# Kernel tuning notes

Measured on AMD Instinct MI355X. Metric: run time of the kernel, lower is better.

Reference implementation:

```python
import jax, jax.numpy as jnp
import numpy as np

B, N, D, H, E = 128, 256, 256, 8, 524288
RATIO = 0.5
HD = D // H
K_SEL = int(N * RATIO)  # nodes kept per graph


def setup_inputs() -> dict:
    key = jax.random.key(0)
    ks = jax.random.split(key, 12)
    embeddings = jax.random.normal(ks[0], (B, N, D), dtype=jnp.float32)
    mask = jnp.ones((B, N), dtype=bool)
    dist = jax.random.uniform(ks[1], (B, N, N), dtype=jnp.float32)
    # within-graph random edges, offset per graph
    epg = E // B
    src = jax.random.randint(ks[2], (B, epg), 0, N)
    dst = jax.random.randint(ks[3], (B, epg), 0, N)
    off = (jnp.arange(B) * N)[:, None]
    edge_index = jnp.stack([(src + off).reshape(-1), (dst + off).reshape(-1)]).astype(jnp.int64)
    batch = jnp.repeat(jnp.arange(B, dtype=jnp.int64), N)
    s = 1.0 / np.sqrt(D)
    Wq = jax.random.normal(ks[4], (D, D), jnp.float32) * s
    Wk = jax.random.normal(ks[5], (D, D), jnp.float32) * s
    Wv = jax.random.normal(ks[6], (D, D), jnp.float32) * s
    Wo = jax.random.normal(ks[7], (D, D), jnp.float32) * s
    bq = jnp.zeros((D,), jnp.float32)
    bk = jnp.zeros((D,), jnp.float32)
    bv = jnp.zeros((D,), jnp.float32)
    bo = jnp.zeros((D,), jnp.float32)
    pool_w = jax.random.normal(ks[8], (D,), jnp.float32) * s
    return dict(embeddings=embeddings, mask=mask, dist=dist, edge_index=edge_index,
                batch=batch, Wq=Wq, bq=bq, Wk=Wk, bk=bk, Wv=Wv, bv=bv, Wo=Wo, bo=bo,
                pool_w=pool_w)


def _mha(x, mask, dist, Wq, bq, Wk, bk, Wv, bv, Wo, bo):
    # x: [B,N,D]; dist used as additive attention bias; mask: [B,N] key mask
    q = (x @ Wq + bq).reshape(B, N, H, HD).transpose(0, 2, 1, 3)  # bhnd
    k = (x @ Wk + bk).reshape(B, N, H, HD).transpose(0, 2, 1, 3)
    v = (x @ Wv + bv).reshape(B, N, H, HD).transpose(0, 2, 1, 3)
    scores = jnp.einsum('bhnd,bhmd->bhnm', q, k) / jnp.sqrt(jnp.float32(HD))
    scores = scores + dist[:, None]  # broadcast bias over heads
    scores = jnp.where(mask[:, None, None, :], scores, jnp.float32(-1e9))
    attn = jax.nn.softmax(scores, axis=-1)
    out = jnp.einsum('bhnm,bhmd->bhnd', attn, v)
    out = out.transpose(0, 2, 1, 3).reshape(B, N, D)
    return out @ Wo + bo


def reference(embeddings, mask, dist, edge_index, batch, Wq, bq, Wk, bk, Wv, bv, Wo, bo, pool_w):
    encoder_result = _mha(embeddings, mask, dist, Wq, bq, Wk, bk, Wv, bv, Wo, bo)
    # encoder_result[mask] -> sparse node features; mask is all-true so shape is [B*N, D]
    x = encoder_result.reshape(B * N, D)

    # ---- TopKPooling (PyG semantics): score = x.w/||w||, keep top ceil(ratio*N)/graph ----
    score = (x @ pool_w) / jnp.linalg.norm(pool_w)          # [B*N]
    vals, idx = jax.lax.top_k(score.reshape(B, N), K_SEL)    # per-graph top-k
    perm = (idx + (jnp.arange(B) * N)[:, None]).reshape(-1)  # [B*K] global node ids
    sub_x = x[perm] * jnp.tanh(vals).reshape(-1, 1)
    sub_batch = batch[perm]

    # relabel nodes: new id = position in perm (PyG ordering); dropped -> sentinel
    n_keep = B * K_SEL
    sentinel = n_keep
    new_id = jnp.full((B * N,), sentinel, dtype=edge_index.dtype).at[perm].set(
        jnp.arange(n_keep, dtype=edge_index.dtype))
    row = new_id[edge_index[0]]
    col = new_id[edge_index[1]]
    valid = (row < sentinel) & (col < sentinel)
    row = jnp.where(valid, row, sentinel)
    col = jnp.where(valid, col, sentinel)
    # sort_edge_index: row-major sort; invalid (sentinel) edges pushed to the end
    order = jnp.argsort(row * (sentinel + 1) + col)
    sub_edge_index = jnp.stack([row, col])[:, order]
    return encoder_result, sub_x, sub_edge_index, sub_batch
```

## Files before the change

### kernel.cpp

```cpp
#include <hip/hip_runtime.h>
#include <math.h>

#define Bg   128
#define Ng   256
#define Dg   256
#define Hg   8
#define HDg  32
#define Eg   524288
#define Kg   128
#define BNg  32768
#define SENT 16384

using bf16x8 = __attribute__((ext_vector_type(8))) short;
using f32x4  = __attribute__((ext_vector_type(4))) float;

__device__ inline void split2(float x, short &h, short &l) {
    unsigned u = __float_as_uint(x);
    h = (short)(u >> 16);
    float hf = __uint_as_float(u & 0xffff0000u);
    float r = x - hf;
    l = (short)(__float_as_uint(r) >> 16);
}
__device__ inline unsigned packsplit(float x) {
    unsigned u = __float_as_uint(x);
    float hf = __uint_as_float(u & 0xffff0000u);
    float r = x - hf;
    unsigned lu = __float_as_uint(r);
    return (u >> 16) | (lu & 0xffff0000u);
}
__device__ inline unsigned pack2(short a, short b) {
    return (unsigned)(unsigned short)a | ((unsigned)(unsigned short)b << 16);
}

__global__ __launch_bounds__(256) void split_x(
    const float* __restrict__ x, short* __restrict__ xh, short* __restrict__ xl)
{
    size_t i = ((size_t)blockIdx.x * 256 + threadIdx.x) * 8;
    float4 a = *(const float4*)(x + i);
    float4 b = *(const float4*)(x + i + 4);
    float v[8] = {a.x,a.y,a.z,a.w,b.x,b.y,b.z,b.w};
    short h[8], l[8];
    #pragma unroll
    for (int j = 0; j < 8; ++j) split2(v[j], h[j], l[j]);
    uint4 uh, ul;
    uh.x = pack2(h[0],h[1]); uh.y = pack2(h[2],h[3]);
    uh.z = pack2(h[4],h[5]); uh.w = pack2(h[6],h[7]);
    ul.x = pack2(l[0],l[1]); ul.y = pack2(l[2],l[3]);
    ul.z = pack2(l[4],l[5]); ul.w = pack2(l[6],l[7]);
    *(uint4*)(xh + i) = uh;
    *(uint4*)(xl + i) = ul;
}

__global__ __launch_bounds__(256) void wprep(
    const float* __restrict__ Wq, const float* __restrict__ Wk,
    const float* __restrict__ Wv, const float* __restrict__ Wo,
    short* __restrict__ WTh, short* __restrict__ WTl)
{
    __shared__ float t[64][65];
    const int bid = blockIdx.x;
    const int mat = bid >> 4;
    const int kt = (bid >> 2) & 3, nt = bid & 3;
    const float* W = (mat==0) ? Wq : (mat==1) ? Wk : (mat==2) ? Wv : Wo;
    const int tid = threadIdx.x;
    const int r = tid >> 2, c4 = tid & 3;
    #pragma unroll
    for (int i = 0; i < 4; ++i) {
        float4 v = *(const float4*)(W + (size_t)(kt*64 + r)*256 + nt*64 + c4*16 + i*4);
        t[r][c4*16 + i*4 + 0] = v.x; t[r][c4*16 + i*4 + 1] = v.y;
        t[r][c4*16 + i*4 + 2] = v.z; t[r][c4*16 + i*4 + 3] = v.w;
    }
    __syncthreads();
    const int n = r, k0 = c4 * 16;
    short hb[16], lb[16];
    #pragma unroll
    for (int i = 0; i < 16; ++i) split2(t[k0 + i][n], hb[i], lb[i]);
    size_t base = (size_t)mat*65536 + (size_t)(nt*64 + n)*256 + kt*64 + k0;
    uint4 uh0, uh1, ul0, ul1;
    uh0.x=pack2(hb[0],hb[1]);  uh0.y=pack2(hb[2],hb[3]);  uh0.z=pack2(hb[4],hb[5]);  uh0.w=pack2(hb[6],hb[7]);
    uh1.x=pack2(hb[8],hb[9]);  uh1.y=pack2(hb[10],hb[11]);uh1.z=pack2(hb[12],hb[13]);uh1.w=pack2(hb[14],hb[15]);
    ul0.x=pack2(lb[0],lb[1]);  ul0.y=pack2(lb[2],lb[3]);  ul0.z=pack2(lb[4],lb[5]);  ul0.w=pack2(lb[6],lb[7]);
    ul1.x=pack2(lb[8],lb[9]);  ul1.y=pack2(lb[10],lb[11]);ul1.z=pack2(lb[12],lb[13]);ul1.w=pack2(lb[14],lb[15]);
    *(uint4*)&WTh[base]     = uh0; *(uint4*)&WTh[base + 8] = uh1;
    *(uint4*)&WTl[base]     = ul0; *(uint4*)&WTl[base + 8] = ul1;
}

__global__ __launch_bounds__(256) void qkv_mm(
    const short* __restrict__ xh, const short* __restrict__ xl,
    const short* __restrict__ WTh, const short* __restrict__ WTl,
    const float* __restrict__ bq, const float* __restrict__ bk, const float* __restrict__ bv,
    unsigned* __restrict__ Qp, unsigned* __restrict__ Kp, unsigned* __restrict__ Vp)
{
    const int z = blockIdx.z;
    const float* bias = (z==0) ? bq : (z==1) ? bk : bv;
    unsigned* out     = (z==0) ? Qp : (z==1) ? Kp : Vp;
    const float scale = (z==0) ? 0.17677669529663687f : 1.0f;
    const short* bth = WTh + (size_t)z * 65536;
    const short* btl = WTl + (size_t)z * 65536;
    __shared__ __align__(16) short lds[16384];
    const int tid = threadIdx.x;
    const int lane = tid & 63, w = tid >> 6;
    const int g = lane >> 4, li = lane & 15;
    const int wr = w >> 1, wc = w & 1;
    const int m0 = blockIdx.x * 128, n0 = blockIdx.y * 128;
    f32x4 acc[4][4];
    #pragma unroll
    for (int i = 0; i < 4; ++i)
        #pragma unroll
        for (int j = 0; j < 4; ++j) acc[i][j] = (f32x4){0.f,0.f,0.f,0.f};

    for (int k0 = 0; k0 < 256; k0 += 32) {
        #pragma unroll
        for (int it = 0; it < 2; ++it) {
            int chunk = it*256 + tid;
            int r = chunk >> 2, c = chunk & 3;
            size_t ga = (size_t)(m0 + r)*256 + k0 + c*8;
            size_t gb = (size_t)(n0 + r)*256 + k0 + c*8;
            uint4 vh = *(const uint4*)(xh + ga);
            uint4 vl = *(const uint4*)(xl + ga);
            uint4 wh = *(const uint4*)(bth + gb);
            uint4 wl = *(const uint4*)(btl + gb);
            *(uint4*)&lds[        chunk*8] = vh;
            *(uint4*)&lds[ 4096 + chunk*8] = vl;
            *(uint4*)&lds[ 8192 + chunk*8] = wh;
            *(uint4*)&lds[12288 + chunk*8] = wl;
        }
        __syncthreads();
        bf16x8 ah[4], al[4], bh[4], bl[4];
        #pragma unroll
        for (int i = 0; i < 4; ++i) {
            int row = wr*64 + i*16 + li;
            ah[i] = *(const bf16x8*)&lds[       row*32 + g*8];
            al[i] = *(const bf16x8*)&lds[4096 + row*32 + g*8];
        }
        #pragma unroll
        for (int j = 0; j < 4; ++j) {
            int row = wc*64 + j*16 + li;
            bh[j] = *(const bf16x8*)&lds[ 8192 + row*32 + g*8];
            bl[j] = *(const bf16x8*)&lds[12288 + row*32 + g*8];
        }
        #pragma unroll
        for (int i = 0; i < 4; ++i)
            #pragma unroll
            for (int j = 0; j < 4; ++j) {
                acc[i][j] = __builtin_amdgcn_mfma_f32_16x16x32_bf16(ah[i], bh[j], acc[i][j], 0,0,0);
                acc[i][j] = __builtin_amdgcn_mfma_f32_16x16x32_bf16(ah[i], bl[j], acc[i][j], 0,0,0);
                acc[i][j] = __builtin_amdgcn_mfma_f32_16x16x32_bf16(al[i], bh[j], acc[i][j], 0,0,0);
                acc[i][j] = __builtin_amdgcn_mfma_f32_16x16x32_bf16(al[i], bl[j], acc[i][j], 0,0,0);
            }
        __syncthreads();
    }
    #pragma unroll
    for (int i = 0; i < 4; ++i)
        #pragma unroll
        for (int j = 0; j < 4; ++j)
            #pragma unroll
            for (int r = 0; r < 4; ++r) {
                int m = m0 + wr*64 + i*16 + g*4 + r;
                int c = n0 + wc*64 + j*16 + li;
                int b = m >> 8, nn = m & 255;
                int h = c >> 5, hd = c & 31;
                float val = (acc[i][j][r] + bias[c]) * scale;
                out[((size_t)(b*Hg + h)*Ng + nn)*HDg + hd] = packsplit(val);
            }
}

__global__ __launch_bounds__(256, 3) void attn_mfma(
    const unsigned* __restrict__ Qp, const unsigned* __restrict__ Kp,
    const unsigned* __restrict__ Vp, const float* __restrict__ dist,
    unsigned* __restrict__ AOp)
{
    __shared__ short    Khi[2][32][40];
    __shared__ short    Klo[2][32][40];
    __shared__ unsigned Vt [2][32][32];
    __shared__ unsigned P32[4][64][32];

    const int i0 = blockIdx.x;
    const int xcd = i0 & 7;
    const int m_  = i0 >> 3;
    const int h   = m_ & 7;
    const int b   = (m_ >> 3) * 8 + xcd;
    const int bh  = b * 8 + h;

    const int tid = threadIdx.x;
    const int w = tid >> 6;
    const int lane = tid & 63;
    const int g = lane >> 4;
    const int li = lane & 15;
    const int r7 = li & 7;
    const int q0 = w * 64;
    const int skey = tid >> 3, se0 = (tid & 7) * 4;
    const float* dall = dist + (size_t)b*Ng*Ng;

    bf16x8 qh[4], ql[4];
    #pragma unroll
    for (int tq = 0; tq < 4; ++tq) {
        const unsigned* qp = Qp + ((size_t)bh * Ng + q0 + tq*16 + li) * HDg + g*8;
        uint4 u0 = *(const uint4*)qp;
        uint4 u1 = *(const uint4*)(qp + 4);
        unsigned uu[8] = {u0.x,u0.y,u0.z,u0.w,u1.x,u1.y,u1.z,u1.w};
        #pragma unroll
        for (int j = 0; j < 8; ++j) {
            qh[tq][j] = (short)(uu[j] & 0xffff);
            ql[tq][j] = (short)(uu[j] >> 16);
        }
    }

    {
        uint4 kv = *(const uint4*)(Kp + ((size_t)bh*Ng + skey) * HDg + se0);
        uint4 vv = *(const uint4*)(Vp + ((size_t)bh*Ng + skey) * HDg + se0);
        unsigned ka[4] = {kv.x,kv.y,kv.z,kv.w};
        unsigned va[4] = {vv.x,vv.y,vv.z,vv.w};
        #pragma unroll
        for (int i = 0; i < 4; ++i) {
            Khi[0][skey][se0+i] = (short)(ka[i] & 0xffff);
            Klo[0][skey][se0+i] = (short)(ka[i] >> 16);
            int row = se0 + i;
            int cs = ((((skey>>2) ^ (row&7)) << 2) | (skey&3));
            Vt[0][row][cs] = va[i];
        }
    }
    __syncthreads();

    f32x4 O[4][2];
    #pragma unroll
    for (int tq=0;tq<4;++tq)
        #pragma unroll
        for (int td=0;td<2;++td) O[tq][td] = (f32x4){0.f,0.f,0.f,0.f};
    float lpart[4] = {0.f, 0.f, 0.f, 0.f};

    for (int ch = 0; ch < 8; ++ch) {
        const int cur = ch & 1;
        const bool pref = (ch < 7);
        uint4 kvr, vvr;
        if (pref) {
            kvr = *(const uint4*)(Kp + ((size_t)bh*Ng + (ch+1)*32 + skey) * HDg + se0);
            vvr = *(const uint4*)(Vp + ((size_t)bh*Ng + (ch+1)*32 + skey) * HDg + se0);
        }
        f32x4 sacc[4][2];
        #pragma unroll
        for (int tq = 0; tq < 4; ++tq)
            #pragma unroll
            for (int tc = 0; tc < 2; ++tc) {
                const float* dp = dall + (size_t)(q0 + tq*16 + li)*Ng + ch*32 + tc*16 + g*4;
                float4 dv = *(const float4*)dp;
                sacc[tq][tc] = (f32x4){dv.x, dv.y, dv.z, dv.w};
            }
        bf16x8 kbh[2], kbl[2];
        #pragma unroll
        for (int tc = 0; tc < 2; ++tc) {
            kbh[tc] = *(const bf16x8*)&Khi[cur][tc*16+li][g*8];
            kbl[tc] = *(const bf16x8*)&Klo[cur][tc*16+li][g*8];
        }
        #pragma unroll
        for (int tq = 0; tq < 4; ++tq)
            #pragma unroll
            for (int tc = 0; tc < 2; ++tc) {
                sacc[tq][tc] = __builtin_amdgcn_mfma_f32_16x16x32_bf16(kbh[tc], qh[tq], sacc[tq][tc], 0,0,0);
                sacc[tq][tc] = __builtin_amdgcn_mfma_f32_16x16x32_bf16(kbl[tc], qh[tq], sacc[tq][tc], 0,0,0);
                sacc[tq][tc] = __builtin_amdgcn_mfma_f32_16x16x32_bf16(kbh[tc], ql[tq], sacc[tq][tc], 0,0,0);
                sacc[tq][tc] = __builtin_amdgcn_mfma_f32_16x16x32_bf16(kbl[tc], ql[tq], sacc[tq][tc], 0,0,0);
            }
        #pragma unroll
        for (int tq = 0; tq < 4; ++tq)
            #pragma unroll
            for (int tc = 0; tc < 2; ++tc) {
                float p0 = __expf(sacc[tq][tc][0] - 16.f);
                float p1 = __expf(sacc[tq][tc][1] - 16.f);
                float p2 = __expf(sacc[tq][tc][2] - 16.f);
                float p3 = __expf(sacc[tq][tc][3] - 16.f);
                lpart[tq] += p0; lpart[tq] += p1; lpart[tq] += p2; lpart[tq] += p3;
                uint4 pw4;
                pw4.x = packsplit(p0); pw4.y = packsplit(p1);
                pw4.z = packsplit(p2); pw4.w = packsplit(p3);
                int slot = (4*tc + g) ^ r7;
                *(uint4*)&P32[w][tq*16 + li][slot << 2] = pw4;
            }
        bf16x8 vbh[2], vbl[2];
        #pragma unroll
        for (int td = 0; td < 2; ++td) {
            unsigned tmp[8];
            *(uint4*)&tmp[0] = *(const uint4*)&Vt[cur][td*16+li][((2*g  ) ^ r7) << 2];
            *(uint4*)&tmp[4] = *(const uint4*)&Vt[cur][td*16+li][((2*g+1) ^ r7) << 2];
            #pragma unroll
            for (int j=0;j<8;++j){ vbh[td][j]=(short)(tmp[j]&0xffff); vbl[td][j]=(short)(tmp[j]>>16); }
        }
        #pragma unroll
        for (int tq = 0; tq < 4; ++tq) {
            unsigned tmp[8];
            *(uint4*)&tmp[0] = *(const uint4*)&P32[w][tq*16+li][((2*g  ) ^ r7) << 2];
            *(uint4*)&tmp[4] = *(const uint4*)&P32[w][tq*16+li][((2*g+1) ^ r7) << 2];
            bf16x8 ph, pl;
            #pragma unroll
            for (int j=0;j<8;++j){ ph[j]=(short)(tmp[j]&0xffff); pl[j]=(short)(tmp[j]>>16); }
            #pragma unroll
            for (int td = 0; td < 2; ++td) {
                O[tq][td] = __builtin_amdgcn_mfma_f32_16x16x32_bf16(vbh[td], ph, O[tq][td], 0,0,0);
                O[tq][td] = __builtin_amdgcn_mfma_f32_16x16x32_bf16(vbl[td], ph, O[tq][td], 0,0,0);
                O[tq][td] = __builtin_amdgcn_mfma_f32_16x16x32_bf16(vbh[td], pl, O[tq][td], 0,0,0);
                O[tq][td] = __builtin_amdgcn_mfma_f32_16x16x32_bf16(vbl[td], pl, O[tq][td], 0,0,0);
            }
        }
        if (pref) {
            const int nb = cur ^ 1;
            unsigned ka[4] = {kvr.x,kvr.y,kvr.z,kvr.w};
            unsigned va[4] = {vvr.x,vvr.y,vvr.z,vvr.w};
            #pragma unroll
            for (int i = 0; i < 4; ++i) {
                Khi[nb][skey][se0+i] = (short)(ka[i] & 0xffff);
                Klo[nb][skey][se0+i] = (short)(ka[i] >> 16);
                int row = se0 + i;
                int cs = ((((skey>>2) ^ (row&7)) << 2) | (skey&3));
                Vt[nb][row][cs] = va[i];
            }
        }
        __syncthreads();
    }
    float inv[4];
    #pragma unroll
    for (int tq = 0; tq < 4; ++tq) {
        float s = lpart[tq];
        s += __shfl_xor(s, 16);
        s += __shfl_xor(s, 32);
        inv[tq] = 1.f / s;
    }
    #pragma unroll
    for (int tq = 0; tq < 4; ++tq)
        #pragma unroll
        for (int td = 0; td < 2; ++td) {
            uint4 o4;
            o4.x = packsplit(O[tq][td][0] * inv[tq]);
            o4.y = packsplit(O[tq][td][1] * inv[tq]);
            o4.z = packsplit(O[tq][td][2] * inv[tq]);
            o4.w = packsplit(O[tq][td][3] * inv[tq]);
            int q = q0 + tq*16 + li;
            int d = h*HDg + td*16 + g*4;
            *(uint4*)&AOp[((size_t)b*Ng + q)*Dg + d] = o4;
        }
}

__global__ __launch_bounds__(256) void out_mm(
    const unsigned* __restrict__ aop,
    const short* __restrict__ bth, const short* __restrict__ btl,
    const float* __restrict__ bo, float* __restrict__ enc)
{
    __shared__ __align__(16) short lds[16384];
    const int tid = threadIdx.x;
    const int lane = tid & 63, w = tid >> 6;
    const int g = lane >> 4, li = lane & 15;
    const int wr = w >> 1, wc = w & 1;
    const int m0 = blockIdx.x * 128, n0 = blockIdx.y * 128;
    f32x4 acc[4][4];
    #pragma unroll
    for (int i = 0; i < 4; ++i)
        #pragma unroll
        for (int j = 0; j < 4; ++j) acc[i][j] = (f32x4){0.f,0.f,0.f,0.f};

    for (int k0 = 0; k0 < 256; k0 += 32) {
        #pragma unroll
        for (int it = 0; it < 2; ++it) {
            int chunk = it*256 + tid;
            int r = chunk >> 2, c = chunk & 3;
            size_t ga = (size_t)(m0 + r)*256 + k0 + c*8;
            size_t gb = (size_t)(n0 + r)*256 + k0 + c*8;
            uint4 p0 = *(const uint4*)(aop + ga);
            uint4 p1 = *(const uint4*)(aop + ga + 4);
            unsigned a[8] = {p0.x,p0.y,p0.z,p0.w,p1.x,p1.y,p1.z,p1.w};
            uint4 hw, lw;
            hw.x = (a[0]&0xffffu)|(a[1]<<16); lw.x = (a[0]>>16)|(a[1]&0xffff0000u);
            hw.y = (a[2]&0xffffu)|(a[3]<<16); lw.y = (a[2]>>16)|(a[3]&0xffff0000u);
            hw.z = (a[4]&0xffffu)|(a[5]<<16); lw.z = (a[4]>>16)|(a[5]&0xffff0000u);
            hw.w = (a[6]&0xffffu)|(a[7]<<16); lw.w = (a[6]>>16)|(a[7]&0xffff0000u);
            uint4 wh = *(const uint4*)(bth + gb);
            uint4 wl = *(const uint4*)(btl + gb);
            *(uint4*)&lds[        chunk*8] = hw;
            *(uint4*)&lds[ 4096 + chunk*8] = lw;
            *(uint4*)&lds[ 8192 + chunk*8] = wh;
            *(uint4*)&lds[12288 + chunk*8] = wl;
        }
        __syncthreads();
        bf16x8 ah[4], al[4], bh[4], bl[4];
        #pragma unroll
        for (int i = 0; i < 4; ++i) {
            int row = wr*64 + i*16 + li;
            ah[i] = *(const bf16x8*)&lds[       row*32 + g*8];
            al[i] = *(const bf16x8*)&lds[4096 + row*32 + g*8];
        }
        #pragma unroll
        for (int j = 0; j < 4; ++j) {
            int row = wc*64 + j*16 + li;
            bh[j] = *(const bf16x8*)&lds[ 8192 + row*32 + g*8];
            bl[j] = *(const bf16x8*)&lds[12288 + row*32 + g*8];
        }
        #pragma unroll
        for (int i = 0; i < 4; ++i)
            #pragma unroll
            for (int j = 0; j < 4; ++j) {
                acc[i][j] = __builtin_amdgcn_mfma_f32_16x16x32_bf16(ah[i], bh[j], acc[i][j], 0,0,0);
                acc[i][j] = __builtin_amdgcn_mfma_f32_16x16x32_bf16(ah[i], bl[j], acc[i][j], 0,0,0);
                acc[i][j] = __builtin_amdgcn_mfma_f32_16x16x32_bf16(al[i], bh[j], acc[i][j], 0,0,0);
                acc[i][j] = __builtin_amdgcn_mfma_f32_16x16x32_bf16(al[i], bl[j], acc[i][j], 0,0,0);
            }
        __syncthreads();
    }
    #pragma unroll
    for (int i = 0; i < 4; ++i)
        #pragma unroll
        for (int j = 0; j < 4; ++j)
            #pragma unroll
            for (int r = 0; r < 4; ++r) {
                int m = m0 + wr*64 + i*16 + g*4 + r;
                int c = n0 + wc*64 + j*16 + li;
                enc[(size_t)m*Dg + c] = acc[i][j][r] + bo[c];
            }
}

__global__ __launch_bounds__(256) void score_kernel(
    const float* __restrict__ enc, const float* __restrict__ pw, float* __restrict__ score)
{
    int row  = blockIdx.x * 8 + (threadIdx.x >> 5);
    int lane = threadIdx.x & 31;
    const float* r = enc + (size_t)row * Dg;
    float s = 0.f;
    for (int d = lane; d < Dg; d += 32) s = fmaf(r[d], pw[d], s);
    #pragma unroll
    for (int off = 16; off > 0; off >>= 1) s += __shfl_xor(s, off);
    if (lane == 0) score[row] = s;
}

__global__ void norm_kernel(const float* __restrict__ pw, float* __restrict__ inv_norm)
{
    int t = threadIdx.x;
    float s = 0.f;
    for (int d = t; d < Dg; d += 64) s = fmaf(pw[d], pw[d], s);
    #pragma unroll
    for (int off = 32; off > 0; off >>= 1) s += __shfl_xor(s, off);
    if (t == 0) *inv_norm = 1.0f / sqrtf(s);
}

__global__ __launch_bounds__(256) void topk_kernel(
    const float* __restrict__ score, float* __restrict__ vals, int* __restrict__ idxs,
    int* __restrict__ new_id, float* __restrict__ out_batch)
{
    __shared__ float sh[Ng];
    int bgr = blockIdx.x, t = threadIdx.x;
    float mine = score[(size_t)bgr * Ng + t];
    sh[t] = mine;
    __syncthreads();
    int cnt = 0;
    for (int j = 0; j < Ng; ++j) {
        float v = sh[j];
        cnt += (v > mine || (v == mine && j < t)) ? 1 : 0;
    }
    if (cnt < Kg) {
        int pos = bgr * Kg + cnt;
        vals[pos] = mine;
        idxs[pos] = t;
        new_id[bgr * Ng + t] = pos;
        out_batch[pos] = (float)bgr;
    } else {
        new_id[bgr * Ng + t] = SENT;
    }
}

__global__ __launch_bounds__(256) void subx_kernel(
    const float* __restrict__ enc, const float* __restrict__ vals,
    const int* __restrict__ idxs, const float* __restrict__ inv_norm,
    float* __restrict__ out_subx)
{
    int j    = blockIdx.x * 4 + (threadIdx.x >> 6);
    int lane = threadIdx.x & 63;
    int bgr  = j >> 7;
    int src  = bgr * Ng + idxs[j];
    float scale = tanhf(vals[j] * (*inv_norm));
    float4 v = reinterpret_cast<const float4*>(enc + (size_t)src * Dg)[lane];
    v.x *= scale; v.y *= scale; v.z *= scale; v.w *= scale;
    reinterpret_cast<float4*>(out_subx + (size_t)j * Dg)[lane] = v;
}

__global__ __launch_bounds__(256) void edge_hist(
    const int* __restrict__ ei, const int* __restrict__ new_id, int* __restrict__ counts)
{
    int e = blockIdx.x * 256 + threadIdx.x;
    int r = new_id[ei[e]];
    int c = new_id[ei[Eg + e]];
    if (r != SENT && c != SENT) atomicAdd(&counts[r], 1);
}

__global__ __launch_bounds__(256) void scan_kernel(
    const int* __restrict__ counts, int* __restrict__ offsets)
{
    __shared__ int sums[256];
    int t = threadIdx.x;
    int base = t * 64;
    int s = 0;
    for (int i = 0; i < 64; ++i) s += counts[base + i];
    sums[t] = s;
    __syncthreads();
    for (int off = 1; off < 256; off <<= 1) {
        int add = (t >= off) ? sums[t - off] : 0;
        __syncthreads();
        sums[t] += add;
        __syncthreads();
    }
    int run = sums[t] - s;
    for (int i = 0; i < 64; ++i) { offsets[base + i] = run; run += counts[base + i]; }
    if (t == 255) offsets[SENT] = run;
}

__global__ __launch_bounds__(256) void edge_scatter(
    const int* __restrict__ ei, const int* __restrict__ new_id,
    const int* __restrict__ offsets, int* __restrict__ cursor, int* __restrict__ bucket)
{
    int e = blockIdx.x * 256 + threadIdx.x;
    int r = new_id[ei[e]];
    int c = new_id[ei[Eg + e]];
    if (r != SENT && c != SENT) {
        int pos = offsets[r] + atomicAdd(&cursor[r], 1);
        bucket[pos] = c;
    }
}

__global__ __launch_bounds__(256) void edge_sort_emit(
    const int* __restrict__ offsets, int* bucket, float* __restrict__ out_edges)
{
    int r = blockIdx.x * 256 + threadIdx.x;
    int s = offsets[r], e = offsets[r + 1];
    for (int i = s + 1; i < e; ++i) {
        int key = bucket[i];
        int j = i - 1;
        while (j >= s && bucket[j] > key) { bucket[j+1] = bucket[j]; --j; }
        bucket[j+1] = key;
    }
    float rf = (float)r;
    for (int i = s; i < e; ++i) {
        out_edges[i]      = rf;
        out_edges[Eg + i] = (float)bucket[i];
    }
}

__global__ __launch_bounds__(256) void edge_fill(
    const int* __restrict__ offsets, float* __restrict__ out_edges)
{
    int p = blockIdx.x * 256 + threadIdx.x;
    if (p >= offsets[SENT]) {
        out_edges[p]      = (float)SENT;
        out_edges[Eg + p] = (float)SENT;
    }
}

extern "C" void kernel_launch(void* const* d_in, const int* in_sizes, int n_in,
                              void* d_out, int out_size, void* d_ws, size_t ws_size,
                              hipStream_t stream)
{
    const float* x    = (const float*)d_in[0];
    const float* dist = (const float*)d_in[2];
    const int*   ei   = (const int*)d_in[3];
    const float* Wq = (const float*)d_in[5];
    const float* bq = (const float*)d_in[6];
    const float* Wk = (const float*)d_in[7];
    const float* bk = (const float*)d_in[8];
    const float* Wv = (const float*)d_in[9];
    const float* bv = (const float*)d_in[10];
    const float* Wo = (const float*)d_in[11];
    const float* bo = (const float*)d_in[12];
    const float* pw = (const float*)d_in[13];

    float* out       = (float*)d_out;
    float* enc_out   = out;
    float* subx_out  = out + 8388608;
    float* edge_out  = out + 12582912;
    float* batch_out = out + 13631488;

    float* ws      = (float*)d_ws;
    unsigned* Qp   = (unsigned*)ws;
    unsigned* Kp   = (unsigned*)(ws + 8388608);
    unsigned* Vp   = (unsigned*)(ws + 16777216);
    short* xh      = (short*)(ws + 25165824);
    short* xl      = (short*)(ws + 29360128);
    unsigned* AOp  = (unsigned*)xh;
    short* WTh     = (short*)(ws + 33554432);
    short* WTl     = (short*)(ws + 33685504);
    float* score   = ws + 33816576;
    float* vals    = ws + 33849344;
    int*   idxs    = (int*)(ws + 33865728);
    int*   new_id  = (int*)(ws + 33882112);
    int*   counts  = (int*)(ws + 33914880);
    int*   offsets = (int*)(ws + 33931264);
    int*   cursor  = (int*)(ws + 33947680);
    float* inv_nm  = ws + 33964064;
    int*   bucket  = (int*)(ws + 33964096);

    hipMemsetAsync(counts, 0, SENT * sizeof(int), stream);
    hipMemsetAsync(cursor, 0, SENT * sizeof(int), stream);

    split_x       <<<dim3(4096),               256, 0, stream>>>(x, xh, xl);
    wprep         <<<dim3(64),                 256, 0, stream>>>(Wq, Wk, Wv, Wo, WTh, WTl);
    norm_kernel   <<<dim3(1),                   64, 0, stream>>>(pw, inv_nm);
    qkv_mm        <<<dim3(BNg/128, Dg/128, 3), 256, 0, stream>>>(xh, xl, WTh, WTl, bq, bk, bv, Qp, Kp, Vp);
    attn_mfma     <<<dim3(Bg*Hg),              256, 0, stream>>>(Qp, Kp, Vp, dist, AOp);
    out_mm        <<<dim3(BNg/128, Dg/128),    256, 0, stream>>>(AOp, WTh + 3*65536, WTl + 3*65536, bo, enc_out);
    score_kernel  <<<dim3(BNg/8),              256, 0, stream>>>(enc_out, pw, score);
    topk_kernel   <<<dim3(Bg),                 256, 0, stream>>>(score, vals, idxs, new_id, batch_out);
    subx_kernel   <<<dim3((Bg*Kg)/4),          256, 0, stream>>>(enc_out, vals, idxs, inv_nm, subx_out);
    edge_hist     <<<dim3(Eg/256),             256, 0, stream>>>(ei, new_id, counts);
    scan_kernel   <<<dim3(1),                  256, 0, stream>>>(counts, offsets);
    edge_scatter  <<<dim3(Eg/256),             256, 0, stream>>>(ei, new_id, offsets, cursor, bucket);
    edge_sort_emit<<<dim3(SENT/256),           256, 0, stream>>>(offsets, bucket, edge_out);
    edge_fill     <<<dim3(Eg/256),             256, 0, stream>>>(offsets, edge_out);
    (void)in_sizes; (void)n_in; (void)out_size; (void)ws_size;
}
```

Before: 242.8 us.

## Drop lo*lo MFMA term and store split bf16 hi/lo planes separately

Removes the low-times-low bf16 MFMA product in all three split-precision GEMMs (QKV, attention QK/PV, output projection), cutting MFMA work by a quarter. Intermediate Q/K/V, P and attention output change from interleaved hi|lo 32-bit packing to separate hi and lo short planes, so the unpacking shuffles are gone and fragments load directly as bf16x8. The attention kernel's LDS layout changes (padded rows, no XOR swizzle, transposed V stored as shorts), and occupancy is lowered to 2 blocks per SM. Dropping the lo*lo term slightly reduces accuracy, and the scalar short stores for transposed V may cause LDS bank conflicts.

After: 241.2 us. Within noise of the previous version (-0.7%).

```diff
diff --git a/kernel.cpp b/kernel.cpp
--- a/kernel.cpp
+++ b/kernel.cpp
@@ -21,13 +21,6 @@
     float r = x - hf;
     l = (short)(__float_as_uint(r) >> 16);
 }
-__device__ inline unsigned packsplit(float x) {
-    unsigned u = __float_as_uint(x);
-    float hf = __uint_as_float(u & 0xffff0000u);
-    float r = x - hf;
-    unsigned lu = __float_as_uint(r);
-    return (u >> 16) | (lu & 0xffff0000u);
-}
 __device__ inline unsigned pack2(short a, short b) {
     return (unsigned)(unsigned short)a | ((unsigned)(unsigned short)b << 16);
 }
@@ -88,11 +81,14 @@
     const short* __restrict__ xh, const short* __restrict__ xl,
     const short* __restrict__ WTh, const short* __restrict__ WTl,
     const float* __restrict__ bq, const float* __restrict__ bk, const float* __restrict__ bv,
-    unsigned* __restrict__ Qp, unsigned* __restrict__ Kp, unsigned* __restrict__ Vp)
+    short* __restrict__ Qh, short* __restrict__ Ql,
+    short* __restrict__ Kh, short* __restrict__ Kl,
+    short* __restrict__ Vh, short* __restrict__ Vl)
 {
     const int z = blockIdx.z;
     const float* bias = (z==0) ? bq : (z==1) ? bk : bv;
-    unsigned* out     = (z==0) ? Qp : (z==1) ? Kp : Vp;
+    short* outH       = (z==0) ? Qh : (z==1) ? Kh : Vh;
+    short* outL       = (z==0) ? Ql : (z==1) ? Kl : Vl;
     const float scale = (z==0) ? 0.17677669529663687f : 1.0f;
     const short* bth = WTh + (size_t)z * 65536;
     const short* btl = WTl + (size_t)z * 65536;
@@ -145,7 +141,6 @@
                 acc[i][j] = __builtin_amdgcn_mfma_f32_16x16x32_bf16(ah[i], bh[j], acc[i][j], 0,0,0);
                 acc[i][j] = __builtin_amdgcn_mfma_f32_16x16x32_bf16(ah[i], bl[j], acc[i][j], 0,0,0);
                 acc[i][j] = __builtin_amdgcn_mfma_f32_16x16x32_bf16(al[i], bh[j], acc[i][j], 0,0,0);
-                acc[i][j] = __builtin_amdgcn_mfma_f32_16x16x32_bf16(al[i], bl[j], acc[i][j], 0,0,0);
             }
         __syncthreads();
     }
@@ -160,19 +155,25 @@
                 int b = m >> 8, nn = m & 255;
                 int h = c >> 5, hd = c & 31;
                 float val = (acc[i][j][r] + bias[c]) * scale;
-                out[((size_t)(b*Hg + h)*Ng + nn)*HDg + hd] = packsplit(val);
-            }
-}
-
-__global__ __launch_bounds__(256, 3) void attn_mfma(
-    const unsigned* __restrict__ Qp, const unsigned* __restrict__ Kp,
-    const unsigned* __restrict__ Vp, const float* __restrict__ dist,
-    unsigned* __restrict__ AOp)
-{
-    __shared__ short    Khi[2][32][40];
-    __shared__ short    Klo[2][32][40];
-    __shared__ unsigned Vt [2][32][32];
-    __shared__ unsigned P32[4][64][32];
+                short hh, ll; split2(val, hh, ll);
+                size_t idx = ((size_t)(b*Hg + h)*Ng + nn)*HDg + hd;
+                outH[idx] = hh; outL[idx] = ll;
+            }
+}
+
+__global__ __launch_bounds__(256, 2) void attn_mfma(
+    const short* __restrict__ Qh, const short* __restrict__ Ql,
+    const short* __restrict__ Kh, const short* __restrict__ Kl,
+    const short* __restrict__ Vh, const short* __restrict__ Vl,
+    const float* __restrict__ dist,
+    short* __restrict__ AOh, short* __restrict__ AOl)
+{
+    __shared__ __align__(16) short Khi [2][32][40];
+    __shared__ __align__(16) short Klo [2][32][40];
+    __shared__ __align__(16) short Vthi[2][32][40];
+    __shared__ __align__(16) short Vtlo[2][32][40];
+    __shared__ __align__(16) short Phi [4][64][40];
+    __shared__ __align__(16) short Plo [4][64][40];
 
     const int i0 = blockIdx.x;
     const int xcd = i0 & 7;
@@ -186,7 +187,6 @@
     const int lane = tid & 63;
     const int g = lane >> 4;
     const int li = lane & 15;
-    const int r7 = li & 7;
     const int q0 = w * 64;
     const int skey = tid >> 3, se0 = (tid & 7) * 4;
     const float* dall = dist + (size_t)b*Ng*Ng;
@@ -194,30 +194,27 @@
     bf16x8 qh[4], ql[4];
     #pragma unroll
     for (int tq = 0; tq < 4; ++tq) {
-        const unsigned* qp = Qp + ((size_t)bh * Ng + q0 + tq*16 + li) * HDg + g*8;
-        uint4 u0 = *(const uint4*)qp;
-        uint4 u1 = *(const uint4*)(qp + 4);
-        unsigned uu[8] = {u0.x,u0.y,u0.z,u0.w,u1.x,u1.y,u1.z,u1.w};
-        #pragma unroll
-        for (int j = 0; j < 8; ++j) {
-            qh[tq][j] = (short)(uu[j] & 0xffff);
-            ql[tq][j] = (short)(uu[j] >> 16);
-        }
+        size_t qoff = ((size_t)bh * Ng + q0 + tq*16 + li) * HDg + g*8;
+        qh[tq] = *(const bf16x8*)(Qh + qoff);
+        ql[tq] = *(const bf16x8*)(Ql + qoff);
     }
 
     {
-        uint4 kv = *(const uint4*)(Kp + ((size_t)bh*Ng + skey) * HDg + se0);
-        uint4 vv = *(const uint4*)(Vp + ((size_t)bh*Ng + skey) * HDg + se0);
-        unsigned ka[4] = {kv.x,kv.y,kv.z,kv.w};
-        unsigned va[4] = {vv.x,vv.y,vv.z,vv.w};
-        #pragma unroll
-        for (int i = 0; i < 4; ++i) {
-            Khi[0][skey][se0+i] = (short)(ka[i] & 0xffff);
-            Klo[0][skey][se0+i] = (short)(ka[i] >> 16);
-            int row = se0 + i;
-            int cs = ((((skey>>2) ^ (row&7)) << 2) | (skey&3));
-            Vt[0][row][cs] = va[i];
-        }
+        size_t koff = ((size_t)bh*Ng + skey) * HDg + se0;
+        uint2 kh2 = *(const uint2*)(Kh + koff);
+        uint2 kl2 = *(const uint2*)(Kl + koff);
+        uint2 vh2 = *(const uint2*)(Vh + koff);
+        uint2 vl2 = *(const uint2*)(Vl + koff);
+        *(uint2*)&Khi[0][skey][se0] = kh2;
+        *(uint2*)&Klo[0][skey][se0] = kl2;
+        Vthi[0][se0+0][skey] = (short)(vh2.x & 0xffff);
+        Vthi[0][se0+1][skey] = (short)(vh2.x >> 16);
+        Vthi[0][se0+2][skey] = (short)(vh2.y & 0xffff);
+        Vthi[0][se0+3][skey] = (short)(vh2.y >> 16);
+        Vtlo[0][se0+0][skey] = (short)(vl2.x & 0xffff);
+        Vtlo[0][se0+1][skey] = (short)(vl2.x >> 16);
+        Vtlo[0][se0+2][skey] = (short)(vl2.y & 0xffff);
+        Vtlo[0][se0+3][skey] = (short)(vl2.y >> 16);
     }
     __syncthreads();
 
@@ -231,10 +228,13 @@
     for (int ch = 0; ch < 8; ++ch) {
         const int cur = ch & 1;
         const bool pref = (ch < 7);
-        uint4 kvr, vvr;
+        uint2 khr, klr, vhr, vlr;
         if (pref) {
-            kvr = *(const uint4*)(Kp + ((size_t)bh*Ng + (ch+1)*32 + skey) * HDg + se0);
-            vvr = *(const uint4*)(Vp + ((size_t)bh*Ng + (ch+1)*32 + skey) * HDg + se0);
+            size_t koff = ((size_t)bh*Ng + (ch+1)*32 + skey) * HDg + se0;
+            khr = *(const uint2*)(Kh + koff);
+            klr = *(const uint2*)(Kl + koff);
+            vhr = *(const uint2*)(Vh + koff);
+            vlr = *(const uint2*)(Vl + koff);
         }
         f32x4 sacc[4][2];
         #pragma unroll
@@ -258,7 +258,6 @@
                 sacc[tq][tc] = __builtin_amdgcn_mfma_f32_16x16x32_bf16(kbh[tc], qh[tq], sacc[tq][tc], 0,0,0);
                 sacc[tq][tc] = __builtin_amdgcn_mfma_f32_16x16x32_bf16(kbl[tc], qh[tq], sacc[tq][tc], 0,0,0);
                 sacc[tq][tc] = __builtin_amdgcn_mfma_f32_16x16x32_bf16(kbh[tc], ql[tq], sacc[tq][tc], 0,0,0);
-                sacc[tq][tc] = __builtin_amdgcn_mfma_f32_16x16x32_bf16(kbl[tc], ql[tq], sacc[tq][tc], 0,0,0);
             }
         #pragma unroll
         for (int tq = 0; tq < 4; ++tq)
@@ -269,49 +268,49 @@
                 float p2 = __expf(sacc[tq][tc][2] - 16.f);
                 float p3 = __expf(sacc[tq][tc][3] - 16.f);
                 lpart[tq] += p0; lpart[tq] += p1; lpart[tq] += p2; lpart[tq] += p3;
-                uint4 pw4;
-                pw4.x = packsplit(p0); pw4.y = packsplit(p1);
-                pw4.z = packsplit(p2); pw4.w = packsplit(p3);
-                int slot = (4*tc + g) ^ r7;
-                *(uint4*)&P32[w][tq*16 + li][slot << 2] = pw4;
+                unsigned u0 = __float_as_uint(p0), u1 = __float_as_uint(p1);
+                unsigned u2 = __float_as_uint(p2), u3 = __float_as_uint(p3);
+                float r0 = p0 - __uint_as_float(u0 & 0xffff0000u);
+                float r1 = p1 - __uint_as_float(u1 & 0xffff0000u);
+                float r2 = p2 - __uint_as_float(u2 & 0xffff0000u);
+                float r3 = p3 - __uint_as_float(u3 & 0xffff0000u);
+                uint2 hiq, loq;
+                hiq.x = (u0 >> 16) | (u1 & 0xffff0000u);
+                hiq.y = (u2 >> 16) | (u3 & 0xffff0000u);
+                loq.x = (__float_as_uint(r0) >> 16) | (__float_as_uint(r1) & 0xffff0000u);
+                loq.y = (__float_as_uint(r2) >> 16) | (__float_as_uint(r3) & 0xffff0000u);
+                *(uint2*)&Phi[w][tq*16 + li][tc*16 + g*4] = hiq;
+                *(uint2*)&Plo[w][tq*16 + li][tc*16 + g*4] = loq;
             }
         bf16x8 vbh[2], vbl[2];
         #pragma unroll
         for (int td = 0; td < 2; ++td) {
-            unsigned tmp[8];
-            *(uint4*)&tmp[0] = *(const uint4*)&Vt[cur][td*16+li][((2*g  ) ^ r7) << 2];
-            *(uint4*)&tmp[4] = *(const uint4*)&Vt[cur][td*16+li][((2*g+1) ^ r7) << 2];
-            #pragma unroll
-            for (int j=0;j<8;++j){ vbh[td][j]=(short)(tmp[j]&0xffff); vbl[td][j]=(short)(tmp[j]>>16); }
+            vbh[td] = *(const bf16x8*)&Vthi[cur][td*16+li][g*8];
+            vbl[td] = *(const bf16x8*)&Vtlo[cur][td*16+li][g*8];
         }
         #pragma unroll
         for (int tq = 0; tq < 4; ++tq) {
-            unsigned tmp[8];
-            *(uint4*)&tmp[0] = *(const uint4*)&P32[w][tq*16+li][((2*g  ) ^ r7) << 2];
-            *(uint4*)&tmp[4] = *(const uint4*)&P32[w][tq*16+li][((2*g+1) ^ r7) << 2];
-            bf16x8 ph, pl;
-            #pragma unroll
-            for (int j=0;j<8;++j){ ph[j]=(short)(tmp[j]&0xffff); pl[j]=(short)(tmp[j]>>16); }
+            bf16x8 ph = *(const bf16x8*)&Phi[w][tq*16+li][g*8];
+            bf16x8 pl = *(const bf16x8*)&Plo[w][tq*16+li][g*8];
             #pragma unroll
             for (int td = 0; td < 2; ++td) {
                 O[tq][td] = __builtin_amdgcn_mfma_f32_16x16x32_bf16(vbh[td], ph, O[tq][td], 0,0,0);
                 O[tq][td] = __builtin_amdgcn_mfma_f32_16x16x32_bf16(vbl[td], ph, O[tq][td], 0,0,0);
                 O[tq][td] = __builtin_amdgcn_mfma_f32_16x16x32_bf16(vbh[td], pl, O[tq][td], 0,0,0);
-                O[tq][td] = __builtin_amdgcn_mfma_f32_16x16x32_bf16(vbl[td], pl, O[tq][td], 0,0,0);
             }
         }
         if (pref) {
             const int nb = cur ^ 1;
-            unsigned ka[4] = {kvr.x,kvr.y,kvr.z,kvr.w};
-            unsigned va[4] = {vvr.x,vvr.y,vvr.z,vvr.w};
-            #pragma unroll
-            for (int i = 0; i < 4; ++i) {
-                Khi[nb][skey][se0+i] = (short)(ka[i] & 0xffff);
-                Klo[nb][skey][se0+i] = (short)(ka[i] >> 16);
-                int row = se0 + i;
-                int cs = ((((skey>>2) ^ (row&7)) << 2) | (skey&3));
-                Vt[nb][row][cs] = va[i];
-            }
+            *(uint2*)&Khi[nb][skey][se0] = khr;
+            *(uint2*)&Klo[nb][skey][se0] = klr;
+            Vthi[nb][se0+0][skey] = (short)(vhr.x & 0xffff);
+            Vthi[nb][se0+1][skey] = (short)(vhr.x >> 16);
+            Vthi[nb][se0+2][skey] = (short)(vhr.y & 0xffff);
+            Vthi[nb][se0+3][skey] = (short)(vhr.y >> 16);
+            Vtlo[nb][se0+0][skey] = (short)(vlr.x & 0xffff);
+            Vtlo[nb][se0+1][skey] = (short)(vlr.x >> 16);
+            Vtlo[nb][se0+2][skey] = (short)(vlr.y & 0xffff);
+            Vtlo[nb][se0+3][skey] = (short)(vlr.y >> 16);
         }
         __syncthreads();
     }
@@ -327,19 +326,30 @@
     for (int tq = 0; tq < 4; ++tq)
         #pragma unroll
         for (int td = 0; td < 2; ++td) {
-            uint4 o4;
-            o4.x = packsplit(O[tq][td][0] * inv[tq]);
-            o4.y = packsplit(O[tq][td][1] * inv[tq]);
-            o4.z = packsplit(O[tq][td][2] * inv[tq]);
-            o4.w = packsplit(O[tq][td][3] * inv[tq]);
+            float v0 = O[tq][td][0] * inv[tq];
+            float v1 = O[tq][td][1] * inv[tq];
+            float v2 = O[tq][td][2] * inv[tq];
+            float v3 = O[tq][td][3] * inv[tq];
+            unsigned u0 = __float_as_uint(v0), u1 = __float_as_uint(v1);
+            unsigned u2 = __float_as_uint(v2), u3 = __float_as_uint(v3);
+            float r0 = v0 - __uint_as_float(u0 & 0xffff0000u);
+            float r1 = v1 - __uint_as_float(u1 & 0xffff0000u);
+            float r2 = v2 - __uint_as_float(u2 & 0xffff0000u);
+            float r3 = v3 - __uint_as_float(u3 & 0xffff0000u);
+            uint2 hiq, loq;
+            hiq.x = (u0 >> 16) | (u1 & 0xffff0000u);
+            hiq.y = (u2 >> 16) | (u3 & 0xffff0000u);
+            loq.x = (__float_as_uint(r0) >> 16) | (__float_as_uint(r1) & 0xffff0000u);
+            loq.y = (__float_as_uint(r2) >> 16) | (__float_as_uint(r3) & 0xffff0000u);
             int q = q0 + tq*16 + li;
-            int d = h*HDg + td*16 + g*4;
-            *(uint4*)&AOp[((size_t)b*Ng + q)*Dg + d] = o4;
+            size_t base = ((size_t)b*Ng + q)*Dg + h*HDg + td*16 + g*4;
+            *(uint2*)&AOh[base] = hiq;
+            *(uint2*)&AOl[base] = loq;
         }
 }
 
 __global__ __launch_bounds__(256) void out_mm(
-    const unsigned* __restrict__ aop,
+    const short* __restrict__ aoh, const short* __restrict__ aol,
     const short* __restrict__ bth, const short* __restrict__ btl,
     const float* __restrict__ bo, float* __restrict__ enc)
 {
@@ -362,18 +372,12 @@
             int r = chunk >> 2, c = chunk & 3;
             size_t ga = (size_t)(m0 + r)*256 + k0 + c*8;
             size_t gb = (size_t)(n0 + r)*256 + k0 + c*8;
-            uint4 p0 = *(const uint4*)(aop + ga);
-            uint4 p1 = *(const uint4*)(aop + ga + 4);
-            unsigned a[8] = {p0.x,p0.y,p0.z,p0.w,p1.x,p1.y,p1.z,p1.w};
-            uint4 hw, lw;
-            hw.x = (a[0]&0xffffu)|(a[1]<<16); lw.x = (a[0]>>16)|(a[1]&0xffff0000u);
-            hw.y = (a[2]&0xffffu)|(a[3]<<16); lw.y = (a[2]>>16)|(a[3]&0xffff0000u);
-            hw.z = (a[4]&0xffffu)|(a[5]<<16); lw.z = (a[4]>>16)|(a[5]&0xffff0000u);
-            hw.w = (a[6]&0xffffu)|(a[7]<<16); lw.w = (a[6]>>16)|(a[7]&0xffff0000u);
-            uint4 wh = *(const uint4*)(bth + gb);
-            uint4 wl = *(const uint4*)(btl + gb);
-            *(uint4*)&lds[        chunk*8] = hw;
-            *(uint4*)&lds[ 4096 + chunk*8] = lw;
+            uint4 ah4 = *(const uint4*)(aoh + ga);
+            uint4 al4 = *(const uint4*)(aol + ga);
+            uint4 wh  = *(const uint4*)(bth + gb);
+            uint4 wl  = *(const uint4*)(btl + gb);
+            *(uint4*)&lds[        chunk*8] = ah4;
+            *(uint4*)&lds[ 4096 + chunk*8] = al4;
             *(uint4*)&lds[ 8192 + chunk*8] = wh;
             *(uint4*)&lds[12288 + chunk*8] = wl;
         }
@@ -398,7 +402,6 @@
                 acc[i][j] = __builtin_amdgcn_mfma_f32_16x16x32_bf16(ah[i], bh[j], acc[i][j], 0,0,0);
                 acc[i][j] = __builtin_amdgcn_mfma_f32_16x16x32_bf16(ah[i], bl[j], acc[i][j], 0,0,0);
                 acc[i][j] = __builtin_amdgcn_mfma_f32_16x16x32_bf16(al[i], bh[j], acc[i][j], 0,0,0);
-                acc[i][j] = __builtin_amdgcn_mfma_f32_16x16x32_bf16(al[i], bl[j], acc[i][j], 0,0,0);
             }
         __syncthreads();
     }
@@ -572,12 +575,16 @@
     float* batch_out = out + 13631488;
 
     float* ws      = (float*)d_ws;
-    unsigned* Qp   = (unsigned*)ws;
-    unsigned* Kp   = (unsigned*)(ws + 8388608);
-    unsigned* Vp   = (unsigned*)(ws + 16777216);
+    short* Qh      = (short*)ws;
+    short* Ql      = (short*)(ws + 4194304);
+    short* Kh      = (short*)(ws + 8388608);
+    short* Kl      = (short*)(ws + 12582912);
+    short* Vh      = (short*)(ws + 16777216);
+    short* Vl      = (short*)(ws + 20971520);
     short* xh      = (short*)(ws + 25165824);
     short* xl      = (short*)(ws + 29360128);
-    unsigned* AOp  = (unsigned*)xh;
+    short* AOh     = xh;
+    short* AOl     = xl;
     short* WTh     = (short*)(ws + 33554432);
     short* WTl     = (short*)(ws + 33685504);
     float* score   = ws + 33816576;
@@ -596,9 +603,10 @@
     split_x       <<<dim3(4096),               256, 0, stream>>>(x, xh, xl);
     wprep         <<<dim3(64),                 256, 0, stream>>>(Wq, Wk, Wv, Wo, WTh, WTl);
     norm_kernel   <<<dim3(1),                   64, 0, stream>>>(pw, inv_nm);
-    qkv_mm        <<<dim3(BNg/128, Dg/128, 3), 256, 0, stream>>>(xh, xl, WTh, WTl, bq, bk, bv, Qp, Kp, Vp);
-    attn_mfma     <<<dim3(Bg*Hg),              256, 0, stream>>>(Qp, Kp, Vp, dist, AOp);
-    out_mm        <<<dim3(BNg/128, Dg/128),    256, 0, stream>>>(AOp, WTh + 3*65536, WTl + 3*65536, bo, enc_out);
+    qkv_mm        <<<dim3(BNg/128, Dg/128, 3), 256, 0, stream>>>(xh, xl, WTh, WTl, bq, bk, bv,
+                                                                 Qh, Ql, Kh, Kl, Vh, Vl);
+    attn_mfma     <<<dim3(Bg*Hg),              256, 0, stream>>>(Qh, Ql, Kh, Kl, Vh, Vl, dist, AOh, AOl);
+    out_mm        <<<dim3(BNg/128, Dg/128),    256, 0, stream>>>(AOh, AOl, WTh + 3*65536, WTl + 3*65536, bo, enc_out);
     score_kernel  <<<dim3(BNg/8),              256, 0, stream>>>(enc_out, pw, score);
     topk_kernel   <<<dim3(Bg),                 256, 0, stream>>>(score, vals, idxs, new_id, batch_out);
     subx_kernel   <<<dim3((Bg*Kg)/4),          256, 0, stream>>>(enc_out, vals, idxs, inv_nm, subx_out);
```
